# Performance work log

Measured on AMD Instinct MI355X. Metric: run time of the kernel, lower is better.

The kernel has to match this reference:

```python
import jax, jax.numpy as jnp
import numpy as np

B, S, H = 1, 2048, 2048
NH, NKV, HD = 16, 2, 128
ROPE_THETA = 1000000.0
BF16 = jnp.bfloat16


def setup_inputs() -> dict:
    key = jax.random.key(0)
    ks = jax.random.split(key, 6)
    hidden_states = jax.random.normal(ks[0], (B, S, H), dtype=jnp.float32)
    # causal additive mask, 0 on/below diagonal, large negative above
    causal = jnp.tril(jnp.ones((S, S), dtype=bool))
    attention_mask = jnp.where(causal, 0.0, -1e9).astype(jnp.float32)[None, None, :, :]
    position_ids = jnp.arange(S, dtype=jnp.int32)[None, :]
    sc = 1.0 / np.sqrt(H)
    Wq = jax.random.normal(ks[1], (H, H), dtype=jnp.float32) * sc
    bq = jnp.zeros((H,), dtype=jnp.float32)
    Wk = jax.random.normal(ks[2], (H, NKV * HD), dtype=jnp.float32) * sc
    bk = jnp.zeros((NKV * HD,), dtype=jnp.float32)
    Wv = jax.random.normal(ks[3], (H, NKV * HD), dtype=jnp.float32) * sc
    bv = jnp.zeros((NKV * HD,), dtype=jnp.float32)
    Wo = jax.random.normal(ks[4], (H, H), dtype=jnp.float32) * sc
    return {"hidden_states": hidden_states, "attention_mask": attention_mask,
            "position_ids": position_ids, "Wq": Wq, "bq": bq, "Wk": Wk, "bk": bk,
            "Wv": Wv, "bv": bv, "Wo": Wo}


def _rope_tables(pos):
    # pos: [S] int. freqs: [HD//2]
    freqs = 1.0 / (ROPE_THETA ** (jnp.arange(0, HD, 2, dtype=jnp.float32) / HD))
    ang = pos.astype(jnp.float32)[:, None] * freqs[None, :]  # [S, HD//2]
    return jnp.cos(ang), jnp.sin(ang)


def _apply_rope(x, cos, sin):
    # x: [B,S,nheads,HD]; cos/sin: [S,HD//2] -> broadcast over heads
    c = cos[None, :, None, :]
    s = sin[None, :, None, :]
    x1, x2 = x[..., : HD // 2], x[..., HD // 2 :]
    return jnp.concatenate([x1 * c - x2 * s, x1 * s + x2 * c], axis=-1)


def reference(hidden_states, attention_mask, position_ids, Wq, bq, Wk, bk, Wv, bv, Wo):
    x = hidden_states.astype(BF16)
    # bf16 projections (flax Dense dtype=bfloat16)
    q = (x @ Wq.astype(BF16) + bq.astype(BF16)).reshape(B, S, NH, HD)
    k = (x @ Wk.astype(BF16) + bk.astype(BF16)).reshape(B, S, NKV, HD)
    v = (x @ Wv.astype(BF16) + bv.astype(BF16)).reshape(B, S, NKV, HD)
    cos, sin = _rope_tables(position_ids[0])
    q = _apply_rope(q.astype(jnp.float32), cos, sin).astype(jnp.float32)
    k = _apply_rope(k.astype(jnp.float32), cos, sin).astype(jnp.float32)
    cache_k, cache_v = k, v  # cache holds un-repeated kv (k post-rope, v bf16)
    rep = NH // NKV  # GQA repeat
    k = jnp.repeat(k, rep, axis=2)
    vr = jnp.repeat(v, rep, axis=2)
    # [B,NH,S,HD]
    qh = q.transpose(0, 2, 1, 3)
    kh = k.transpose(0, 2, 1, 3)
    vh = vr.transpose(0, 2, 1, 3).astype(jnp.float32)
    scale = 1.0 / jnp.sqrt(jnp.float32(HD))
    scores = jnp.einsum('bhqd,bhkd->bhqk', qh, kh) * scale + attention_mask
    probs = jnp.clip(jax.nn.softmax(scores.astype(jnp.float32), axis=-1), 1e-09, 1 - 1e-09)
    attn = jnp.einsum('bhqk,bhkd->bhqd', probs, vh)
    attn = attn.transpose(0, 2, 1, 3).reshape(B, S, H)
    out = (attn.astype(BF16) @ Wo.astype(BF16)).astype(jnp.float32)
    return out, cache_k, cache_v
```

## Files before the change

kernel.cpp:

```cpp
#include <hip/hip_runtime.h>
#include <hip/hip_bf16.h>
#include <math.h>

#define S_LEN 2048
#define HDIM  2048
#define N_H   16
#define N_KV  2
#define HD_   128
#define NQKV  2560

typedef __attribute__((ext_vector_type(8))) short bf16x8;
typedef __attribute__((ext_vector_type(4))) float f32x4;
typedef __attribute__((ext_vector_type(16))) float f32x16;

#define GLDS16(gsrc, ldst)                                                      \
  __builtin_amdgcn_global_load_lds(                                             \
      (const __attribute__((address_space(1))) void*)(gsrc),                    \
      (__attribute__((address_space(3))) void*)(ldst), 16, 0, 0)

__device__ __forceinline__ ushort f2b(float x) {
  union { __hip_bfloat16 b; ushort u; } c;
  c.b = __float2bfloat16(x);
  return c.u;
}
__device__ __forceinline__ float b2f(ushort u) {
  union { float f; unsigned v; } c;
  c.v = ((unsigned)u) << 16;
  return c.f;
}
__device__ __forceinline__ uint pk2(float a, float b) {
  return (uint)f2b(a) | ((uint)f2b(b) << 16);
}

__global__ __launch_bounds__(256) void k_f32_to_bf16(const float* __restrict__ src,
                                                     ushort* __restrict__ dst, int n4) {
  int i = blockIdx.x * 256 + threadIdx.x;
  if (i >= n4) return;
  float4 v = ((const float4*)src)[i];
  ushort4 o;
  o.x = f2b(v.x); o.y = f2b(v.y); o.z = f2b(v.z); o.w = f2b(v.w);
  ((ushort4*)dst)[i] = o;
}

__global__ __launch_bounds__(256) void k_transpose_bf16(const float* __restrict__ src,
                                                        ushort* __restrict__ dst,
                                                        int R, int C) {
  __shared__ float t[64][65];
  int c0 = blockIdx.x * 64, r0 = blockIdx.y * 64;
  int tx = threadIdx.x & 63, ty = threadIdx.x >> 6;
#pragma unroll
  for (int i = 0; i < 16; ++i)
    t[i * 4 + ty][tx] = src[(size_t)(r0 + i * 4 + ty) * C + (c0 + tx)];
  __syncthreads();
#pragma unroll
  for (int i = 0; i < 16; ++i)
    dst[(size_t)(c0 + i * 4 + ty) * R + (r0 + tx)] = f2b(t[tx][i * 4 + ty]);
}

template <int OUT_MODE>
__global__ __launch_bounds__(256) void k_gemm_bt(const ushort* __restrict__ A,
                                                 const ushort* __restrict__ Bt,
                                                 void* __restrict__ Cp,
                                                 const float* __restrict__ bq,
                                                 const float* __restrict__ bk,
                                                 const float* __restrict__ bv,
                                                 int M, int N, int K) {
  __shared__ ushort lA[128 * 32];
  __shared__ ushort lB[64 * 32];
  const int tid = threadIdx.x;
  const int w = tid >> 6, lane = tid & 63;
  const int lr = lane & 15, lg = lane >> 4;
  const int bm = blockIdx.x * 128, bn = blockIdx.y * 64;
  const int wm = (w >> 1) * 64, wn = (w & 1) * 32;
  f32x4 acc[4][2] = {};

  for (int k0 = 0; k0 < K; k0 += 32) {
    __syncthreads();
#pragma unroll
    for (int it = 0; it < 2; ++it) {
      const int idx = it * 256 + tid;
      const int row = idx >> 2;
      const int kc = (idx & 3) * 8;
      GLDS16(A + (size_t)(bm + row) * K + k0 + kc, lA + (it * 4 + w) * 512);
    }
    {
      const int row = tid >> 2;
      const int kc = (tid & 3) * 8;
      GLDS16(Bt + (size_t)(bn + row) * K + k0 + kc, lB + w * 512);
    }
    __syncthreads();
    bf16x8 af[4], bf[2];
#pragma unroll
    for (int i = 0; i < 4; ++i)
      af[i] = *(const bf16x8*)(lA + (wm + i * 16 + lr) * 32 + lg * 8);
#pragma unroll
    for (int i = 0; i < 2; ++i)
      bf[i] = *(const bf16x8*)(lB + (wn + i * 16 + lr) * 32 + lg * 8);
    __builtin_amdgcn_s_setprio(1);
#pragma unroll
    for (int mi = 0; mi < 4; ++mi)
#pragma unroll
      for (int ni = 0; ni < 2; ++ni)
        acc[mi][ni] =
            __builtin_amdgcn_mfma_f32_16x16x32_bf16(af[mi], bf[ni], acc[mi][ni], 0, 0, 0);
    __builtin_amdgcn_s_setprio(0);
  }

#pragma unroll
  for (int mi = 0; mi < 4; ++mi)
#pragma unroll
    for (int ni = 0; ni < 2; ++ni)
#pragma unroll
      for (int r = 0; r < 4; ++r) {
        const int row = bm + wm + mi * 16 + lg * 4 + r;
        const int col = bn + wn + ni * 16 + lr;
        const float v = acc[mi][ni][r];
        if (OUT_MODE == 0) {
          float bias = (col < 2048) ? bq[col] : (col < 2304 ? bk[col - 2048] : bv[col - 2304]);
          float vb = b2f(f2b(v)) + b2f(f2b(bias));
          ((ushort*)Cp)[(size_t)row * N + col] = f2b(vb);
        } else {
          ((float*)Cp)[(size_t)row * N + col] = b2f(f2b(v));
        }
      }
}

__global__ __launch_bounds__(256) void k_rope(const ushort* __restrict__ qkv,
                                              const int* __restrict__ pos_ids,
                                              ushort* __restrict__ q_r,
                                              ushort* __restrict__ k_r,
                                              ushort* __restrict__ v_t,
                                              float* __restrict__ cache_k,
                                              float* __restrict__ cache_v) {
  const int s = blockIdx.x;
  const int t = threadIdx.x;
  const int i = t & 63, g = t >> 6;
  const float SCALE = 0.08838834764831845f;
  const float pos = (float)pos_ids[s];
  const float freq = (float)(1.0 / pow(1000000.0, (double)i / 64.0));
  float sn, cs;
  sincosf(pos * freq, &sn, &cs);
  const ushort* row = qkv + (size_t)s * NQKV;

#pragma unroll
  for (int j = 0; j < 4; ++j) {
    const int h = j * 4 + g;
    const float x1 = b2f(row[h * 128 + i]);
    const float x2 = b2f(row[h * 128 + 64 + i]);
    const float o1 = x1 * cs - x2 * sn;
    const float o2 = x1 * sn + x2 * cs;
    const size_t qo = ((size_t)h * S_LEN + s) * 128;
    q_r[qo + i] = f2b(o1 * SCALE);
    q_r[qo + 64 + i] = f2b(o2 * SCALE);
  }
  if (g < 2) {
    const int kv = g;
    const float x1 = b2f(row[2048 + kv * 128 + i]);
    const float x2 = b2f(row[2048 + kv * 128 + 64 + i]);
    const float o1 = x1 * cs - x2 * sn;
    const float o2 = x1 * sn + x2 * cs;
    const size_t ko = ((size_t)kv * S_LEN + s) * 128;
    k_r[ko + i] = f2b(o1);
    k_r[ko + 64 + i] = f2b(o2);
    const size_t co = ((size_t)s * 2 + kv) * 128;
    cache_k[co + i] = o1;
    cache_k[co + 64 + i] = o2;
  }
  {
    const int kv = t >> 7, d = t & 127;
    const ushort bits = row[2304 + kv * 128 + d];
    cache_v[((size_t)s * 2 + kv) * 128 + d] = b2f(bits);
    v_t[((size_t)kv * 128 + d) * S_LEN + s] = bits;
  }
}

__global__ __launch_bounds__(256, 2) void k_attn(const ushort* __restrict__ q_r,
                                                 const ushort* __restrict__ k_r,
                                                 const ushort* __restrict__ v_t,
                                                 ushort* __restrict__ attn_b) {
  __shared__ ushort smem[2][2][8192];
  __shared__ float stats[2][32][2];

  const int bi = blockIdx.x;
  const int dir = (bi ^ (bi >> 3)) & 1;
  const int t4 = ((bi >> 1) & 3) | (((bi >> 4) & 3) << 2);
  const int h = ((bi >> 3) & 1) | (((bi >> 6) & 7) << 1);
  const int Q = dir ? (31 - t4) : t4;
  const int kvh = h >> 3;

  const int tid = threadIdx.x, w = tid >> 6, lane = tid & 63;
  const int g = w >> 1, wq = w & 1, tg = tid & 127;
  const int l31 = lane & 31, hb = lane >> 5;
  const int NT = Q + 1;
  const int qmaxw = Q * 64 + wq * 32 + 31;
  const int S_steps = (Q + 2) >> 1;

  bf16x8 qf[8];
  {
    const ushort* qp =
        q_r + ((size_t)(h * S_LEN + Q * 64 + wq * 32 + l31)) * 128 + hb * 8;
#pragma unroll
    for (int f = 0; f < 8; ++f) qf[f] = *(const bf16x8*)(qp + f * 16);
  }

  f32x16 acc[4] = {};
  float m = -INFINITY, l = 0.f;

  for (int s = 0; s < S_steps; ++s) {
    const int t = 2 * s + g;
    const bool have = (t < NT);
    if (have) {
      const int kb = t * 64;
#pragma unroll
      for (int it = 0; it < 8; ++it) {
        const int idx = it * 128 + tg;
        {
          const int key = idx >> 4, sl = idx & 15;
          GLDS16(k_r + ((size_t)(kvh * S_LEN + kb + key)) * 128 + ((sl ^ (key & 7)) * 8),
                 &smem[g][0][it * 1024 + wq * 512]);
        }
        {
          const int d = idx >> 3, sl = idx & 7;
          GLDS16(v_t + ((size_t)(kvh * HD_ + d)) * S_LEN + kb + ((sl ^ (d & 7)) * 8),
                 &smem[g][1][it * 1024 + wq * 512]);
        }
      }
    }
    __syncthreads();

    const int kb = t * 64;
    if (have && kb <= qmaxw) {
      const ushort* lKb = &smem[g][0][0];
      const ushort* lVb = &smem[g][1][0];

      f32x16 p0 = {}, p1 = {};
      __builtin_amdgcn_s_setprio(1);
#pragma unroll
      for (int f = 0; f < 8; ++f) {
        const int key0 = l31;
        const bf16x8 k0 = *(const bf16x8*)(lKb + key0 * 128 + (((2 * f + hb) ^ (key0 & 7)) * 8));
        p0 = __builtin_amdgcn_mfma_f32_32x32x16_bf16(k0, qf[f], p0, 0, 0, 0);
      }
#pragma unroll
      for (int f = 0; f < 8; ++f) {
        const int key1 = 32 + l31;
        const bf16x8 k1 = *(const bf16x8*)(lKb + key1 * 128 + (((2 * f + hb) ^ (key1 & 7)) * 8));
        p1 = __builtin_amdgcn_mfma_f32_32x32x16_bf16(k1, qf[f], p1, 0, 0, 0);
      }
      __builtin_amdgcn_s_setprio(0);

      const int q = Q * 64 + wq * 32 + l31;
      float sv[32];
#pragma unroll
      for (int r = 0; r < 16; ++r) {
        const int key = kb + (r & 3) + 8 * (r >> 2) + 4 * hb;
        sv[r] = (key <= q) ? p0[r] : -INFINITY;
      }
#pragma unroll
      for (int r = 0; r < 16; ++r) {
        const int key = kb + 32 + (r & 3) + 8 * (r >> 2) + 4 * hb;
        sv[16 + r] = (key <= q) ? p1[r] : -INFINITY;
      }
      float tmx[16];
#pragma unroll
      for (int j = 0; j < 16; ++j) tmx[j] = fmaxf(sv[j], sv[j + 16]);
#pragma unroll
      for (int st = 8; st >= 1; st >>= 1)
#pragma unroll
        for (int j = 0; j < 8; ++j)
          if (j < st) tmx[j] = fmaxf(tmx[j], tmx[j + st]);
      const float mxw = fmaxf(tmx[0], __shfl_xor(tmx[0], 32));

      if (__any(mxw > m + 8.f)) {
        const float mn = fmaxf(m, mxw);
        const float sc = __expf(m - mn);
#pragma unroll
        for (int g2 = 0; g2 < 4; ++g2)
#pragma unroll
          for (int r = 0; r < 16; ++r) acc[g2][r] *= sc;
        l *= sc;
        m = mn;
      }
      float ts[16];
#pragma unroll
      for (int r = 0; r < 32; ++r) sv[r] = __expf(sv[r] - m);
#pragma unroll
      for (int j = 0; j < 16; ++j) ts[j] = sv[j] + sv[j + 16];
#pragma unroll
      for (int st = 8; st >= 1; st >>= 1)
#pragma unroll
        for (int j = 0; j < 8; ++j)
          if (j < st) ts[j] += ts[j + st];
      l += ts[0];

      uint pk8[2][8];
#pragma unroll
      for (int j = 0; j < 8; ++j) {
        pk8[0][j] = pk2(sv[2 * j], sv[2 * j + 1]);
        pk8[1][j] = pk2(sv[16 + 2 * j], sv[16 + 2 * j + 1]);
      }
      union FragU { uint wd[4]; bf16x8 v; };
      FragU frag[4];
#pragma unroll
      for (int gg = 0; gg < 2; ++gg)
#pragma unroll
        for (int c1 = 0; c1 < 2; ++c1) {
          uint mine0, mine1, rcv0, rcv1;
          {
            const uint pa = pk8[gg][0 + 4 * c1];
            const uint pb = pk8[gg][2 + 4 * c1];
            const uint mn_ = hb ? pb : pa;
            const uint xc_ = hb ? pa : pb;
            mine0 = mn_;
            rcv0 = (uint)__shfl_xor((int)xc_, 32);
          }
          {
            const uint pa = pk8[gg][1 + 4 * c1];
            const uint pb = pk8[gg][3 + 4 * c1];
            const uint mn_ = hb ? pb : pa;
            const uint xc_ = hb ? pa : pb;
            mine1 = mn_;
            rcv1 = (uint)__shfl_xor((int)xc_, 32);
          }
          const int c = 2 * gg + c1;
          frag[c].wd[0] = hb ? rcv0 : mine0;
          frag[c].wd[1] = hb ? rcv1 : mine1;
          frag[c].wd[2] = hb ? mine0 : rcv0;
          frag[c].wd[3] = hb ? mine1 : rcv1;
        }

      __builtin_amdgcn_s_setprio(1);
#pragma unroll
      for (int g2 = 0; g2 < 4; ++g2) {
        const int d = g2 * 32 + l31;
#pragma unroll
        for (int c = 0; c < 4; ++c) {
          const bf16x8 vf = *(const bf16x8*)(lVb + d * 64 + (((2 * c + hb) ^ (d & 7)) * 8));
          acc[g2] = __builtin_amdgcn_mfma_f32_32x32x16_bf16(vf, frag[c].v, acc[g2], 0, 0, 0);
        }
      }
      __builtin_amdgcn_s_setprio(0);
    }
    __syncthreads();
  }

  float* mrg = (float*)&smem[0][0][0];
  float* ldsO = (float*)&smem[1][0][0];
  if (g == 1) {
    const float lt1 = l + __shfl_xor(l, 32);
#pragma unroll
    for (int g2 = 0; g2 < 4; ++g2)
#pragma unroll
      for (int r = 0; r < 16; ++r) {
        const int d5 = (r & 3) + 8 * (r >> 2) + 4 * hb;
        mrg[wq * 4096 + (g2 * 32 + d5) * 32 + l31] = acc[g2][r];
      }
    if (hb == 0) {
      stats[wq][l31][0] = m;
      stats[wq][l31][1] = lt1;
    }
  }
  __syncthreads();
  if (g == 0) {
    const float m1 = stats[wq][l31][0];
    const float l1 = stats[wq][l31][1];
    const float l0 = l + __shfl_xor(l, 32);
    const float ms = fmaxf(m, m1);
    const float f0 = __expf(m - ms);
    const float f1 = __expf(m1 - ms);
    const float inv = 1.0f / (l0 * f0 + l1 * f1);
#pragma unroll
    for (int g2 = 0; g2 < 4; ++g2)
#pragma unroll
      for (int r = 0; r < 16; ++r) {
        const int d5 = (r & 3) + 8 * (r >> 2) + 4 * hb;
        const float o1v = mrg[wq * 4096 + (g2 * 32 + d5) * 32 + l31];
        const float val = (acc[g2][r] * f0 + o1v * f1) * inv;
        ldsO[wq * 4096 + l31 * 128 + g2 * 32 + (d5 ^ l31)] = val;
      }
#pragma unroll
    for (int pass = 0; pass < 8; ++pass) {
      const int qrow = pass * 4 + (lane >> 4);
      const int d0 = (lane & 15) * 8;
      float v[8];
#pragma unroll
      for (int j = 0; j < 8; ++j)
        v[j] = ldsO[wq * 4096 + qrow * 128 + (((d0 + j) & 31) ^ qrow) + (d0 & 96)];
      uint4 o;
      o.x = pk2(v[0], v[1]); o.y = pk2(v[2], v[3]);
      o.z = pk2(v[4], v[5]); o.w = pk2(v[6], v[7]);
      const size_t qg = (size_t)(Q * 64 + wq * 32 + qrow);
      *(uint4*)(attn_b + qg * HDIM + h * 128 + d0) = o;
    }
  }
}

extern "C" void kernel_launch(void* const* d_in, const int* in_sizes, int n_in,
                              void* d_out, int out_size, void* d_ws, size_t ws_size,
                              hipStream_t stream) {
  const float* hidden = (const float*)d_in[0];
  const int* pos_ids = (const int*)d_in[2];
  const float* Wq = (const float*)d_in[3];
  const float* bq = (const float*)d_in[4];
  const float* Wk = (const float*)d_in[5];
  const float* bk = (const float*)d_in[6];
  const float* Wv = (const float*)d_in[7];
  const float* bv = (const float*)d_in[8];
  const float* Wo = (const float*)d_in[9];

  float* out = (float*)d_out;
  float* cache_k = out + (size_t)S_LEN * HDIM;
  float* cache_v = cache_k + (size_t)S_LEN * N_KV * HD_;

  char* ws = (char*)d_ws;
  ushort* x_b = (ushort*)(ws);
  ushort* wt = (ushort*)(ws + (8u << 20));
  ushort* qkv = (ushort*)(ws + (18u << 20));
  ushort* q_r = (ushort*)(ws);
  ushort* k_r = (ushort*)(ws + (8u << 20));
  ushort* v_t = (ushort*)(ws + (9u << 20));
  ushort* wo_t = (ushort*)(ws + (10u << 20));
  ushort* attn_b = (ushort*)(ws + (18u << 20));

  k_f32_to_bf16<<<dim3((S_LEN * HDIM) / 1024), 256, 0, stream>>>(hidden, x_b,
                                                                 (S_LEN * HDIM) / 4);
  k_transpose_bf16<<<dim3(32, 32), 256, 0, stream>>>(Wq, wt, 2048, 2048);
  k_transpose_bf16<<<dim3(4, 32), 256, 0, stream>>>(Wk, wt + (size_t)2048 * 2048, 2048, 256);
  k_transpose_bf16<<<dim3(4, 32), 256, 0, stream>>>(Wv, wt + (size_t)2304 * 2048, 2048, 256);
  k_gemm_bt<0><<<dim3(16, 40), 256, 0, stream>>>(x_b, wt, qkv, bq, bk, bv, 2048, 2560, 2048);
  k_transpose_bf16<<<dim3(32, 32), 256, 0, stream>>>(Wo, wo_t, 2048, 2048);
  k_rope<<<dim3(S_LEN), 256, 0, stream>>>(qkv, pos_ids, q_r, k_r, v_t, cache_k, cache_v);
  k_attn<<<dim3(512), 256, 0, stream>>>(q_r, k_r, v_t, attn_b);
  k_gemm_bt<1><<<dim3(16, 32), 256, 0, stream>>>(attn_b, wo_t, out, nullptr, nullptr,
                                                 nullptr, 2048, 2048, 2048);
}
```

Before: 168.9 us.

## Split-K GEMMs with 128x128 tiles, fused bias epilogue, double-buffered 32-key attention

Both projection GEMMs now use 128x128 block tiles and a split-K of two, writing bf16 partials. The partials are summed with bias inside the rope kernel, or in a new add-round kernel for the output projection. The attention kernel moves from 64-key single-buffered tiles to 32-key double-buffered K/V staging with one barrier per step, and uses a simpler block-to-(head, query tile) mapping. The aim is to raise MFMA reuse per tile, overlap loads with compute, and cut barriers. In exchange it adds extra partial-sum traffic and launches. Rounding each partial to bf16 before summing also changes numerics slightly.

```diff
diff --git a/kernel.cpp b/kernel.cpp
--- a/kernel.cpp
+++ b/kernel.cpp
@@ -57,50 +57,43 @@
     dst[(size_t)(c0 + i * 4 + ty) * R + (r0 + tx)] = f2b(t[tx][i * 4 + ty]);
 }
 
-template <int OUT_MODE>
 __global__ __launch_bounds__(256) void k_gemm_bt(const ushort* __restrict__ A,
                                                  const ushort* __restrict__ Bt,
-                                                 void* __restrict__ Cp,
-                                                 const float* __restrict__ bq,
-                                                 const float* __restrict__ bk,
-                                                 const float* __restrict__ bv,
-                                                 int M, int N, int K) {
+                                                 ushort* __restrict__ Cp,
+                                                 int M, int N, int Kfull, int Khalf) {
   __shared__ ushort lA[128 * 32];
-  __shared__ ushort lB[64 * 32];
+  __shared__ ushort lB[128 * 32];
   const int tid = threadIdx.x;
   const int w = tid >> 6, lane = tid & 63;
   const int lr = lane & 15, lg = lane >> 4;
-  const int bm = blockIdx.x * 128, bn = blockIdx.y * 64;
-  const int wm = (w >> 1) * 64, wn = (w & 1) * 32;
-  f32x4 acc[4][2] = {};
-
-  for (int k0 = 0; k0 < K; k0 += 32) {
+  const int bm = blockIdx.x * 128, bn = blockIdx.y * 128;
+  const int wm = (w >> 1) * 64, wn = (w & 1) * 64;
+  const int kbeg = blockIdx.z * Khalf;
+  ushort* Cout = Cp + (size_t)blockIdx.z * M * N;
+  f32x4 acc[4][4] = {};
+
+  for (int k0 = kbeg; k0 < kbeg + Khalf; k0 += 32) {
     __syncthreads();
 #pragma unroll
     for (int it = 0; it < 2; ++it) {
       const int idx = it * 256 + tid;
       const int row = idx >> 2;
       const int kc = (idx & 3) * 8;
-      GLDS16(A + (size_t)(bm + row) * K + k0 + kc, lA + (it * 4 + w) * 512);
-    }
-    {
-      const int row = tid >> 2;
-      const int kc = (tid & 3) * 8;
-      GLDS16(Bt + (size_t)(bn + row) * K + k0 + kc, lB + w * 512);
+      GLDS16(A + (size_t)(bm + row) * Kfull + k0 + kc, lA + (it * 4 + w) * 512);
+      GLDS16(Bt + (size_t)(bn + row) * Kfull + k0 + kc, lB + (it * 4 + w) * 512);
     }
     __syncthreads();
-    bf16x8 af[4], bf[2];
-#pragma unroll
-    for (int i = 0; i < 4; ++i)
+    bf16x8 af[4], bf[4];
+#pragma unroll
+    for (int i = 0; i < 4; ++i) {
       af[i] = *(const bf16x8*)(lA + (wm + i * 16 + lr) * 32 + lg * 8);
-#pragma unroll
-    for (int i = 0; i < 2; ++i)
       bf[i] = *(const bf16x8*)(lB + (wn + i * 16 + lr) * 32 + lg * 8);
+    }
     __builtin_amdgcn_s_setprio(1);
 #pragma unroll
     for (int mi = 0; mi < 4; ++mi)
 #pragma unroll
-      for (int ni = 0; ni < 2; ++ni)
+      for (int ni = 0; ni < 4; ++ni)
         acc[mi][ni] =
             __builtin_amdgcn_mfma_f32_16x16x32_bf16(af[mi], bf[ni], acc[mi][ni], 0, 0, 0);
     __builtin_amdgcn_s_setprio(0);
@@ -109,44 +102,58 @@
 #pragma unroll
   for (int mi = 0; mi < 4; ++mi)
 #pragma unroll
-    for (int ni = 0; ni < 2; ++ni)
+    for (int ni = 0; ni < 4; ++ni)
 #pragma unroll
       for (int r = 0; r < 4; ++r) {
         const int row = bm + wm + mi * 16 + lg * 4 + r;
         const int col = bn + wn + ni * 16 + lr;
-        const float v = acc[mi][ni][r];
-        if (OUT_MODE == 0) {
-          float bias = (col < 2048) ? bq[col] : (col < 2304 ? bk[col - 2048] : bv[col - 2304]);
-          float vb = b2f(f2b(v)) + b2f(f2b(bias));
-          ((ushort*)Cp)[(size_t)row * N + col] = f2b(vb);
-        } else {
-          ((float*)Cp)[(size_t)row * N + col] = b2f(f2b(v));
-        }
-      }
-}
-
-__global__ __launch_bounds__(256) void k_rope(const ushort* __restrict__ qkv,
-                                              const int* __restrict__ pos_ids,
-                                              ushort* __restrict__ q_r,
-                                              ushort* __restrict__ k_r,
-                                              ushort* __restrict__ v_t,
-                                              float* __restrict__ cache_k,
-                                              float* __restrict__ cache_v) {
+        Cout[(size_t)row * N + col] = f2b(acc[mi][ni][r]);
+      }
+}
+
+__global__ __launch_bounds__(256) void k_epirope(const ushort* __restrict__ p0,
+                                                 const ushort* __restrict__ p1,
+                                                 const float* __restrict__ bq,
+                                                 const float* __restrict__ bk,
+                                                 const float* __restrict__ bv,
+                                                 const int* __restrict__ pos_ids,
+                                                 ushort* __restrict__ q_r,
+                                                 ushort* __restrict__ k_r,
+                                                 ushort* __restrict__ v_t,
+                                                 float* __restrict__ cache_k,
+                                                 float* __restrict__ cache_v) {
   const int s = blockIdx.x;
   const int t = threadIdx.x;
+  __shared__ float row[NQKV];
+  const uint* a = (const uint*)(p0 + (size_t)s * NQKV);
+  const uint* b = (const uint*)(p1 + (size_t)s * NQKV);
+#pragma unroll
+  for (int j = 0; j < 5; ++j) {
+    const int c2 = t + 256 * j;
+    const uint u0 = a[c2], u1 = b[c2];
+    const int c = 2 * c2;
+    const float v0 = b2f((ushort)u0) + b2f((ushort)(u1 & 0xffff));
+    const float v1 = b2f((ushort)(u0 >> 16)) + b2f((ushort)(u1 >> 16));
+    const float bias0 = (c < 2048) ? bq[c] : (c < 2304 ? bk[c - 2048] : bv[c - 2304]);
+    const float bias1 = (c + 1 < 2048) ? bq[c + 1]
+                                       : (c + 1 < 2304 ? bk[c + 1 - 2048] : bv[c + 1 - 2304]);
+    row[c] = b2f(f2b(b2f(f2b(v0)) + b2f(f2b(bias0))));
+    row[c + 1] = b2f(f2b(b2f(f2b(v1)) + b2f(f2b(bias1))));
+  }
+  __syncthreads();
+
   const int i = t & 63, g = t >> 6;
   const float SCALE = 0.08838834764831845f;
   const float pos = (float)pos_ids[s];
   const float freq = (float)(1.0 / pow(1000000.0, (double)i / 64.0));
   float sn, cs;
   sincosf(pos * freq, &sn, &cs);
-  const ushort* row = qkv + (size_t)s * NQKV;
 
 #pragma unroll
   for (int j = 0; j < 4; ++j) {
     const int h = j * 4 + g;
-    const float x1 = b2f(row[h * 128 + i]);
-    const float x2 = b2f(row[h * 128 + 64 + i]);
+    const float x1 = row[h * 128 + i];
+    const float x2 = row[h * 128 + 64 + i];
     const float o1 = x1 * cs - x2 * sn;
     const float o2 = x1 * sn + x2 * cs;
     const size_t qo = ((size_t)h * S_LEN + s) * 128;
@@ -155,8 +162,8 @@
   }
   if (g < 2) {
     const int kv = g;
-    const float x1 = b2f(row[2048 + kv * 128 + i]);
-    const float x2 = b2f(row[2048 + kv * 128 + 64 + i]);
+    const float x1 = row[2048 + kv * 128 + i];
+    const float x2 = row[2048 + kv * 128 + 64 + i];
     const float o1 = x1 * cs - x2 * sn;
     const float o2 = x1 * sn + x2 * cs;
     const size_t ko = ((size_t)kv * S_LEN + s) * 128;
@@ -168,10 +175,23 @@
   }
   {
     const int kv = t >> 7, d = t & 127;
-    const ushort bits = row[2304 + kv * 128 + d];
-    cache_v[((size_t)s * 2 + kv) * 128 + d] = b2f(bits);
-    v_t[((size_t)kv * 128 + d) * S_LEN + s] = bits;
-  }
+    const float vval = row[2304 + kv * 128 + d];
+    cache_v[((size_t)s * 2 + kv) * 128 + d] = vval;
+    v_t[((size_t)kv * 128 + d) * S_LEN + s] = f2b(vval);
+  }
+}
+
+__global__ __launch_bounds__(256) void k_addround(const ushort* __restrict__ p0,
+                                                  const ushort* __restrict__ p1,
+                                                  float* __restrict__ out, int n2) {
+  int i = blockIdx.x * 256 + threadIdx.x;
+  if (i >= n2) return;
+  const uint a = ((const uint*)p0)[i];
+  const uint b = ((const uint*)p1)[i];
+  float2 o;
+  o.x = b2f(f2b(b2f((ushort)(a & 0xffff)) + b2f((ushort)(b & 0xffff))));
+  o.y = b2f(f2b(b2f((ushort)(a >> 16)) + b2f((ushort)(b >> 16))));
+  ((float2*)out)[i] = o;
 }
 
 __global__ __launch_bounds__(256, 2) void k_attn(const ushort* __restrict__ q_r,
@@ -182,18 +202,16 @@
   __shared__ float stats[2][32][2];
 
   const int bi = blockIdx.x;
-  const int dir = (bi ^ (bi >> 3)) & 1;
-  const int t4 = ((bi >> 1) & 3) | (((bi >> 4) & 3) << 2);
-  const int h = ((bi >> 3) & 1) | (((bi >> 6) & 7) << 1);
-  const int Q = dir ? (31 - t4) : t4;
+  const int h = bi & 15;
+  const int tq = (bi >> 4) & 15;
+  const int Q = (bi >> 8) ? (31 - tq) : tq;
   const int kvh = h >> 3;
 
   const int tid = threadIdx.x, w = tid >> 6, lane = tid & 63;
   const int g = w >> 1, wq = w & 1, tg = tid & 127;
   const int l31 = lane & 31, hb = lane >> 5;
-  const int NT = Q + 1;
+  const int S_steps = Q + 1;
   const int qmaxw = Q * 64 + wq * 32 + 31;
-  const int S_steps = (Q + 2) >> 1;
 
   bf16x8 qf[8];
   {
@@ -206,70 +224,65 @@
   f32x16 acc[4] = {};
   float m = -INFINITY, l = 0.f;
 
+#define STAGE(BUF, T32)                                                           \
+  do {                                                                            \
+    const int kb_ = (T32) * 32;                                                   \
+    _Pragma("unroll") for (int i = 0; i < 4; ++i) {                               \
+      const int idx = i * 128 + tg;                                               \
+      {                                                                           \
+        const int key = idx >> 4, sl = idx & 15;                                  \
+        GLDS16(k_r + ((size_t)(kvh * S_LEN + kb_ + key)) * 128 +                  \
+                   ((sl ^ (key & 7)) * 8),                                        \
+               &smem[g][BUF][i * 1024 + wq * 512]);                               \
+      }                                                                           \
+      {                                                                           \
+        const int d = idx >> 2, p = idx & 3;                                      \
+        const int gs = (p - (d >> 1)) & 3;                                        \
+        GLDS16(v_t + ((size_t)(kvh * HD_ + d)) * S_LEN + kb_ + gs * 8,            \
+               &smem[g][BUF][4096 + i * 1024 + wq * 512]);                        \
+      }                                                                           \
+    }                                                                             \
+  } while (0)
+
+  STAGE(0, g);
+  int buf = 0;
+
   for (int s = 0; s < S_steps; ++s) {
-    const int t = 2 * s + g;
-    const bool have = (t < NT);
-    if (have) {
-      const int kb = t * 64;
-#pragma unroll
-      for (int it = 0; it < 8; ++it) {
-        const int idx = it * 128 + tg;
-        {
-          const int key = idx >> 4, sl = idx & 15;
-          GLDS16(k_r + ((size_t)(kvh * S_LEN + kb + key)) * 128 + ((sl ^ (key & 7)) * 8),
-                 &smem[g][0][it * 1024 + wq * 512]);
-        }
-        {
-          const int d = idx >> 3, sl = idx & 7;
-          GLDS16(v_t + ((size_t)(kvh * HD_ + d)) * S_LEN + kb + ((sl ^ (d & 7)) * 8),
-                 &smem[g][1][it * 1024 + wq * 512]);
-        }
-      }
-    }
     __syncthreads();
-
-    const int kb = t * 64;
-    if (have && kb <= qmaxw) {
-      const ushort* lKb = &smem[g][0][0];
-      const ushort* lVb = &smem[g][1][0];
-
-      f32x16 p0 = {}, p1 = {};
+    if (s + 1 < S_steps) STAGE(buf ^ 1, 2 * (s + 1) + g);
+    const int kb = (2 * s + g) * 32;
+
+    if (kb <= qmaxw) {
+      const ushort* lK = &smem[g][buf][0];
+      const ushort* lV = &smem[g][buf][4096];
+
+      f32x16 p0 = {};
       __builtin_amdgcn_s_setprio(1);
 #pragma unroll
       for (int f = 0; f < 8; ++f) {
-        const int key0 = l31;
-        const bf16x8 k0 = *(const bf16x8*)(lKb + key0 * 128 + (((2 * f + hb) ^ (key0 & 7)) * 8));
-        p0 = __builtin_amdgcn_mfma_f32_32x32x16_bf16(k0, qf[f], p0, 0, 0, 0);
-      }
-#pragma unroll
-      for (int f = 0; f < 8; ++f) {
-        const int key1 = 32 + l31;
-        const bf16x8 k1 = *(const bf16x8*)(lKb + key1 * 128 + (((2 * f + hb) ^ (key1 & 7)) * 8));
-        p1 = __builtin_amdgcn_mfma_f32_32x32x16_bf16(k1, qf[f], p1, 0, 0, 0);
+        const int key = l31;
+        const bf16x8 kf8 =
+            *(const bf16x8*)(lK + key * 128 + (((2 * f + hb) ^ (key & 7)) * 8));
+        p0 = __builtin_amdgcn_mfma_f32_32x32x16_bf16(kf8, qf[f], p0, 0, 0, 0);
       }
       __builtin_amdgcn_s_setprio(0);
 
       const int q = Q * 64 + wq * 32 + l31;
-      float sv[32];
+      float sv[16];
 #pragma unroll
       for (int r = 0; r < 16; ++r) {
         const int key = kb + (r & 3) + 8 * (r >> 2) + 4 * hb;
         sv[r] = (key <= q) ? p0[r] : -INFINITY;
       }
-#pragma unroll
-      for (int r = 0; r < 16; ++r) {
-        const int key = kb + 32 + (r & 3) + 8 * (r >> 2) + 4 * hb;
-        sv[16 + r] = (key <= q) ? p1[r] : -INFINITY;
-      }
-      float tmx[16];
-#pragma unroll
-      for (int j = 0; j < 16; ++j) tmx[j] = fmaxf(sv[j], sv[j + 16]);
-#pragma unroll
-      for (int st = 8; st >= 1; st >>= 1)
-#pragma unroll
-        for (int j = 0; j < 8; ++j)
-          if (j < st) tmx[j] = fmaxf(tmx[j], tmx[j + st]);
-      const float mxw = fmaxf(tmx[0], __shfl_xor(tmx[0], 32));
+      float t8[8];
+#pragma unroll
+      for (int j = 0; j < 8; ++j) t8[j] = fmaxf(sv[j], sv[j + 8]);
+#pragma unroll
+      for (int st = 4; st >= 1; st >>= 1)
+#pragma unroll
+        for (int j = 0; j < 4; ++j)
+          if (j < st) t8[j] = fmaxf(t8[j], t8[j + st]);
+      const float mxw = fmaxf(t8[0], __shfl_xor(t8[0], 32));
 
       if (__any(mxw > m + 8.f)) {
         const float mn = fmaxf(m, mxw);
@@ -281,68 +294,64 @@
         l *= sc;
         m = mn;
       }
-      float ts[16];
-#pragma unroll
-      for (int r = 0; r < 32; ++r) sv[r] = __expf(sv[r] - m);
-#pragma unroll
-      for (int j = 0; j < 16; ++j) ts[j] = sv[j] + sv[j + 16];
-#pragma unroll
-      for (int st = 8; st >= 1; st >>= 1)
-#pragma unroll
-        for (int j = 0; j < 8; ++j)
+#pragma unroll
+      for (int r = 0; r < 16; ++r) sv[r] = __expf(sv[r] - m);
+      float ts[8];
+#pragma unroll
+      for (int j = 0; j < 8; ++j) ts[j] = sv[j] + sv[j + 8];
+#pragma unroll
+      for (int st = 4; st >= 1; st >>= 1)
+#pragma unroll
+        for (int j = 0; j < 4; ++j)
           if (j < st) ts[j] += ts[j + st];
       l += ts[0];
 
-      uint pk8[2][8];
-#pragma unroll
-      for (int j = 0; j < 8; ++j) {
-        pk8[0][j] = pk2(sv[2 * j], sv[2 * j + 1]);
-        pk8[1][j] = pk2(sv[16 + 2 * j], sv[16 + 2 * j + 1]);
-      }
+      uint pk8[8];
+#pragma unroll
+      for (int j = 0; j < 8; ++j) pk8[j] = pk2(sv[2 * j], sv[2 * j + 1]);
       union FragU { uint wd[4]; bf16x8 v; };
-      FragU frag[4];
-#pragma unroll
-      for (int gg = 0; gg < 2; ++gg)
-#pragma unroll
-        for (int c1 = 0; c1 < 2; ++c1) {
-          uint mine0, mine1, rcv0, rcv1;
-          {
-            const uint pa = pk8[gg][0 + 4 * c1];
-            const uint pb = pk8[gg][2 + 4 * c1];
-            const uint mn_ = hb ? pb : pa;
-            const uint xc_ = hb ? pa : pb;
-            mine0 = mn_;
-            rcv0 = (uint)__shfl_xor((int)xc_, 32);
-          }
-          {
-            const uint pa = pk8[gg][1 + 4 * c1];
-            const uint pb = pk8[gg][3 + 4 * c1];
-            const uint mn_ = hb ? pb : pa;
-            const uint xc_ = hb ? pa : pb;
-            mine1 = mn_;
-            rcv1 = (uint)__shfl_xor((int)xc_, 32);
-          }
-          const int c = 2 * gg + c1;
-          frag[c].wd[0] = hb ? rcv0 : mine0;
-          frag[c].wd[1] = hb ? rcv1 : mine1;
-          frag[c].wd[2] = hb ? mine0 : rcv0;
-          frag[c].wd[3] = hb ? mine1 : rcv1;
+      FragU frag[2];
+#pragma unroll
+      for (int c1 = 0; c1 < 2; ++c1) {
+        uint mine0, mine1, rcv0, rcv1;
+        {
+          const uint pa = pk8[0 + 4 * c1];
+          const uint pb = pk8[2 + 4 * c1];
+          const uint mn_ = hb ? pb : pa;
+          const uint xc_ = hb ? pa : pb;
+          mine0 = mn_;
+          rcv0 = (uint)__shfl_xor((int)xc_, 32);
         }
+        {
+          const uint pa = pk8[1 + 4 * c1];
+          const uint pb = pk8[3 + 4 * c1];
+          const uint mn_ = hb ? pb : pa;
+          const uint xc_ = hb ? pa : pb;
+          mine1 = mn_;
+          rcv1 = (uint)__shfl_xor((int)xc_, 32);
+        }
+        frag[c1].wd[0] = hb ? rcv0 : mine0;
+        frag[c1].wd[1] = hb ? rcv1 : mine1;
+        frag[c1].wd[2] = hb ? mine0 : rcv0;
+        frag[c1].wd[3] = hb ? mine1 : rcv1;
+      }
 
       __builtin_amdgcn_s_setprio(1);
 #pragma unroll
       for (int g2 = 0; g2 < 4; ++g2) {
         const int d = g2 * 32 + l31;
 #pragma unroll
-        for (int c = 0; c < 4; ++c) {
-          const bf16x8 vf = *(const bf16x8*)(lVb + d * 64 + (((2 * c + hb) ^ (d & 7)) * 8));
+        for (int c = 0; c < 2; ++c) {
+          const int phys = ((2 * c + hb) + (d >> 1)) & 3;
+          const bf16x8 vf = *(const bf16x8*)(lV + d * 32 + phys * 8);
           acc[g2] = __builtin_amdgcn_mfma_f32_32x32x16_bf16(vf, frag[c].v, acc[g2], 0, 0, 0);
         }
       }
       __builtin_amdgcn_s_setprio(0);
     }
-    __syncthreads();
-  }
+    buf ^= 1;
+  }
+  __syncthreads();
 
   float* mrg = (float*)&smem[0][0][0];
   float* ldsO = (float*)&smem[1][0][0];
@@ -393,6 +402,7 @@
       *(uint4*)(attn_b + qg * HDIM + h * 128 + d0) = o;
     }
   }
+#undef STAGE
 }
 
 extern "C" void kernel_launch(void* const* d_in, const int* in_sizes, int n_in,
@@ -414,23 +424,26 @@
 
   char* ws = (char*)d_ws;
   ushort* x_b = (ushort*)(ws);
-  ushort* wt = (ushort*)(ws + (8u << 20));
-  ushort* qkv = (ushort*)(ws + (18u << 20));
-  ushort* q_r = (ushort*)(ws);
-  ushort* k_r = (ushort*)(ws + (8u << 20));
-  ushort* v_t = (ushort*)(ws + (9u << 20));
-  ushort* wo_t = (ushort*)(ws + (10u << 20));
-  ushort* attn_b = (ushort*)(ws + (18u << 20));
+  ushort* wt = (ushort*)(ws + (8ull << 20));
+  ushort* qkvp = (ushort*)(ws + (18ull << 20));
+  ushort* wo_t = (ushort*)(ws);
+  ushort* q_r = (ushort*)(ws + (8ull << 20));
+  ushort* k_r = (ushort*)(ws + (16ull << 20));
+  ushort* v_t = (ushort*)(ws + (17ull << 20));
+  ushort* attn_b = (ushort*)(ws + (18ull << 20));
+  ushort* outp = (ushort*)(ws + (26ull << 20));
 
   k_f32_to_bf16<<<dim3((S_LEN * HDIM) / 1024), 256, 0, stream>>>(hidden, x_b,
                                                                  (S_LEN * HDIM) / 4);
   k_transpose_bf16<<<dim3(32, 32), 256, 0, stream>>>(Wq, wt, 2048, 2048);
   k_transpose_bf16<<<dim3(4, 32), 256, 0, stream>>>(Wk, wt + (size_t)2048 * 2048, 2048, 256);
   k_transpose_bf16<<<dim3(4, 32), 256, 0, stream>>>(Wv, wt + (size_t)2304 * 2048, 2048, 256);
-  k_gemm_bt<0><<<dim3(16, 40), 256, 0, stream>>>(x_b, wt, qkv, bq, bk, bv, 2048, 2560, 2048);
+  k_gemm_bt<<<dim3(16, 20, 2), 256, 0, stream>>>(x_b, wt, qkvp, 2048, 2560, 2048, 1024);
   k_transpose_bf16<<<dim3(32, 32), 256, 0, stream>>>(Wo, wo_t, 2048, 2048);
-  k_rope<<<dim3(S_LEN), 256, 0, stream>>>(qkv, pos_ids, q_r, k_r, v_t, cache_k, cache_v);
+  k_epirope<<<dim3(S_LEN), 256, 0, stream>>>(qkvp, qkvp + (size_t)2048 * 2560, bq, bk, bv,
+                                             pos_ids, q_r, k_r, v_t, cache_k, cache_v);
   k_attn<<<dim3(512), 256, 0, stream>>>(q_r, k_r, v_t, attn_b);
-  k_gemm_bt<1><<<dim3(16, 32), 256, 0, stream>>>(attn_b, wo_t, out, nullptr, nullptr,
-                                                 nullptr, 2048, 2048, 2048);
-}
+  k_gemm_bt<<<dim3(16, 16, 2), 256, 0, stream>>>(attn_b, wo_t, outp, 2048, 2048, 2048, 1024);
+  k_addround<<<dim3((2048 * 2048 / 2 + 255) / 256), 256, 0, stream>>>(
+      outp, outp + (size_t)2048 * 2048, out, 2048 * 2048 / 2);
+}
```

Result: faster. 158.9 us (-5.9%).
